# Optimization experiments

Hardware: AMD Instinct MI355X
Metric: run time of the kernel (lower is better)

The kernel has to match this reference:

```python
import math
import jax, jax.numpy as jnp
import numpy as np

B, T, D = 2, 1024, 512
H, DK = 8, 64


def setup_inputs() -> dict:
    key = jax.random.key(0)
    ks = jax.random.split(key, 7)
    s = 1.0 / math.sqrt(D)
    x = jax.random.normal(ks[0], (B, T, D), dtype=jnp.float32)
    Wq = jax.random.normal(ks[1], (D, H * DK), dtype=jnp.float32) * s
    Wk = jax.random.normal(ks[2], (D, H * DK), dtype=jnp.float32) * s
    Wv = jax.random.normal(ks[3], (D, H * DK), dtype=jnp.float32) * s
    Wo = jax.random.normal(ks[4], (H * DK, D), dtype=jnp.float32) * s
    Wg = jax.random.normal(ks[5], (D, H * DK), dtype=jnp.float32) * 0.02
    bg = jnp.ones((H * DK,), dtype=jnp.float32)  # gate_bias_init = 1.0
    return {"x": x, "Wq": Wq, "Wk": Wk, "Wv": Wv, "Wo": Wo, "Wg": Wg, "bg": bg}


def reference(x, Wq, Wk, Wv, Wo, Wg, bg):
    b, t, d = x.shape
    Q = jax.nn.relu(x @ Wq).reshape(b, t, H, DK)
    K = jax.nn.relu(x @ Wk).reshape(b, t, H, DK)
    V = (x @ Wv).reshape(b, t, H, DK)
    angle = jnp.arange(t, dtype=x.dtype) * (math.pi / (2 * t))  # (T,)
    cosw = jnp.cos(angle)[None, :, None, None]
    sinw = jnp.sin(angle)[None, :, None, None]
    Qc, Qs = Q * cosw, Q * sinw
    Kc, Ks = K * cosw, K * sinw
    # cumulative KV outer products: (B,T,H,DK,DK)
    Sc = jnp.cumsum(jnp.einsum('bthd,bthe->bthde', Kc, V), axis=1)
    Ss = jnp.cumsum(jnp.einsum('bthd,bthe->bthde', Ks, V), axis=1)
    o = jnp.einsum('bthd,bthde->bthe', Qc, Sc) + jnp.einsum('bthd,bthde->bthe', Qs, Ss)
    zc = jnp.cumsum(Kc, axis=1)
    zs = jnp.cumsum(Ks, axis=1)
    z = jnp.einsum('bthd,bthd->bth', Qc, zc) + jnp.einsum('bthd,bthd->bth', Qs, zs)
    z = jnp.maximum(z, 1e-6)[..., None]
    o = o / z
    gate = jax.nn.sigmoid((x @ Wg + bg).reshape(b, t, H, DK))
    o = o * gate
    return o.reshape(b, t, H * DK) @ Wo
```

## Files before the change

### kernel.cpp

```cpp
#include <hip/hip_runtime.h>
#include <math.h>

#define B_ 2
#define T_ 1024
#define D_ 512
#define H_ 8
#define DK_ 64
#define NBH_ 16
#define C_ 32
#define G_ 32

#define PI_OVER_2T 0.00153398078788564122971808758949f

typedef float f32x4 __attribute__((ext_vector_type(4)));
typedef short s16x8 __attribute__((ext_vector_type(8)));

__device__ __forceinline__ ushort f2bf(float x) {
    unsigned u = __float_as_uint(x);
    unsigned r = (u + 0x7fffu + ((u >> 16) & 1u)) >> 16;
    return (ushort)r;
}
__device__ __forceinline__ float bf2f(ushort u) {
    return __uint_as_float((unsigned)u << 16);
}
__device__ __forceinline__ s16x8 bscale(s16x8 v, float s) {
    s16x8 r;
#pragma unroll
    for (int u = 0; u < 8; u++)
        r[u] = (short)f2bf(bf2f((ushort)v[u]) * s);
    return r;
}

__device__ __forceinline__ void async16(void* lds, const void* g) {
    __builtin_amdgcn_global_load_lds(
        (const __attribute__((address_space(1))) void*)g,
        (__attribute__((address_space(3))) void*)lds, 16, 0, 0);
}

__global__ __launch_bounds__(256) void k_conv(
    const float* __restrict__ x,
    const float* __restrict__ Wq, const float* __restrict__ Wk,
    const float* __restrict__ Wv, const float* __restrict__ Wg,
    const float* __restrict__ Wo,
    ushort* __restrict__ xb, ushort* __restrict__ WtAll)
{
    __shared__ float Ts[64][65];
    const int bx = blockIdx.x;
    const int tid = threadIdx.x;
    if (bx < 1024) {
        int i = (bx * 256 + tid) * 4;
        float4 v = *(const float4*)&x[i];
        ushort4 o;
        o.x = f2bf(v.x); o.y = f2bf(v.y); o.z = f2bf(v.z); o.w = f2bf(v.w);
        *(ushort4*)&xb[i] = o;
        return;
    }
    const int bid = bx - 1024;
    const int mi = bid >> 6;
    const int t64 = bid & 63;
    const float* __restrict__ W = (mi == 0) ? Wq : (mi == 1) ? Wk
                                 : (mi == 2) ? Wv : (mi == 3) ? Wg : Wo;
    const int tr = t64 >> 3, tc = t64 & 7;
#pragma unroll
    for (int p = 0; p < 4; p++) {
        int row = p * 16 + (tid >> 4);
        int c4 = (tid & 15) * 4;
        float4 v = *(const float4*)&W[(size_t)(tr * 64 + row) * 512 + tc * 64 + c4];
        Ts[row][c4 + 0] = v.x; Ts[row][c4 + 1] = v.y;
        Ts[row][c4 + 2] = v.z; Ts[row][c4 + 3] = v.w;
    }
    __syncthreads();
    const int nl = tid >> 2, kc = (tid & 3) * 16;
    ushort buf[16];
#pragma unroll
    for (int u = 0; u < 16; u++) buf[u] = f2bf(Ts[kc + u][nl]);
    ushort* dst = WtAll + (size_t)mi * 262144 + (size_t)(tc * 64 + nl) * 512
                  + tr * 64 + kc;
    *(uint4*)dst = *(uint4*)&buf[0];
    *(uint4*)(dst + 8) = *(uint4*)&buf[8];
}

template<int MODE, int TM, int TN, int BK>
__global__ __launch_bounds__(256) void k_gemm(
    const ushort* __restrict__ A, const ushort* __restrict__ Bt,
    const float* __restrict__ bg,
    void* __restrict__ O0v, void* __restrict__ O1v,
    void* __restrict__ O2v, void* __restrict__ O3v)
{
    constexpr int WM = TM / 2, WN = TN / 2;
    constexpr int FM = WM / 16, FN = WN / 16;
    constexpr int CH = BK / 8;
    constexpr int SH = (BK == 32) ? 1 : 0;
    constexpr int KS = BK / 32;
    constexpr int NA = TM * BK / 2048;
    constexpr int NB = TN * BK / 2048;

    __shared__ ushort As[2][TM * BK];
    __shared__ ushort Bs[2][TN * BK];

    const int tid = threadIdx.x;
    const int ct = blockIdx.x;
    const int rowBase = blockIdx.y * TM;

    const ushort* __restrict__ Bmat;
    int which = 0, matCol;
    if (MODE == 0) {
        which = ct / (512 / TN);
        matCol = (ct % (512 / TN)) * TN;
        Bmat = Bt + (size_t)which * 262144;
    } else {
        matCol = ct * TN;
        Bmat = Bt;
    }

    const int wave = tid >> 6, lane = tid & 63;
    const int q = lane >> 4, ln = lane & 15;
    const int mB = (wave >> 1) * WM, nB = (wave & 1) * WN;

    int fuA[NA], fuB[NB];
    const ushort* gA[NA];
    const ushort* gB[NB];
#pragma unroll
    for (int u = 0; u < NA; u++) {
        int fu = tid * 8 + u * 2048;
        int r = fu / BK;
        int slot = (fu >> 3) & (CH - 1);
        int gc = slot ^ ((r >> SH) & (CH - 1));
        fuA[u] = fu;
        gA[u] = A + (size_t)(rowBase + r) * 512 + gc * 8;
    }
#pragma unroll
    for (int u = 0; u < NB; u++) {
        int fu = tid * 8 + u * 2048;
        int r = fu / BK;
        int slot = (fu >> 3) & (CH - 1);
        int gc = slot ^ ((r >> SH) & (CH - 1));
        fuB[u] = fu;
        gB[u] = Bmat + (size_t)(matCol + r) * 512 + gc * 8;
    }

    f32x4 acc[FM][FN];
#pragma unroll
    for (int i = 0; i < FM; i++)
#pragma unroll
        for (int j = 0; j < FN; j++) acc[i][j] = (f32x4){0.f, 0.f, 0.f, 0.f};

    int aoff[FM][KS], boff[FN][KS];
#pragma unroll
    for (int i = 0; i < FM; i++) {
        int ra = mB + i * 16 + ln;
#pragma unroll
        for (int ks = 0; ks < KS; ks++)
            aoff[i][ks] = ra * BK
                + (((ks * 4 + q) ^ ((ra >> SH) & (CH - 1))) * 8);
    }
#pragma unroll
    for (int j = 0; j < FN; j++) {
        int rb = nB + j * 16 + ln;
#pragma unroll
        for (int ks = 0; ks < KS; ks++)
            boff[j][ks] = rb * BK
                + (((ks * 4 + q) ^ ((rb >> SH) & (CH - 1))) * 8);
    }

#pragma unroll
    for (int u = 0; u < NA; u++) async16(&As[0][fuA[u]], gA[u]);
#pragma unroll
    for (int u = 0; u < NB; u++) async16(&Bs[0][fuB[u]], gB[u]);

    int cur = 0;
    for (int kb = 0; kb < 512; kb += BK) {
        __syncthreads();
        if (kb + BK < 512) {
#pragma unroll
            for (int u = 0; u < NA; u++)
                async16(&As[cur ^ 1][fuA[u]], gA[u] + kb + BK);
#pragma unroll
            for (int u = 0; u < NB; u++)
                async16(&Bs[cur ^ 1][fuB[u]], gB[u] + kb + BK);
        }
#pragma unroll
        for (int ks = 0; ks < KS; ks++) {
            s16x8 af[FM], bf[FN];
#pragma unroll
            for (int i = 0; i < FM; i++)
                af[i] = *(const s16x8*)&As[cur][aoff[i][ks]];
#pragma unroll
            for (int j = 0; j < FN; j++)
                bf[j] = *(const s16x8*)&Bs[cur][boff[j][ks]];
#pragma unroll
            for (int i = 0; i < FM; i++)
#pragma unroll
                for (int j = 0; j < FN; j++)
                    acc[i][j] = __builtin_amdgcn_mfma_f32_16x16x32_bf16(
                        af[i], bf[j], acc[i][j], 0, 0, 0);
        }
        cur ^= 1;
    }

    if (MODE == 0) {
        ushort* __restrict__ Out = (which == 0) ? (ushort*)O0v
                                  : (which == 1) ? (ushort*)O1v
                                  : (which == 2) ? (ushort*)O2v : (ushort*)O3v;
#pragma unroll
        for (int i = 0; i < FM; i++)
#pragma unroll
            for (int j = 0; j < FN; j++) {
                int col = matCol + nB + j * 16 + ln;
#pragma unroll
                for (int r = 0; r < 4; r++) {
                    int row = rowBase + mB + i * 16 + q * 4 + r;
                    float v = acc[i][j][r];
                    if (which <= 1) v = fmaxf(v, 0.f);
                    else if (which == 3) v = 1.f / (1.f + expf(-(v + bg[col])));
                    Out[(size_t)row * 512 + col] = f2bf(v);
                }
            }
    } else {
        float* __restrict__ Out = (float*)O0v;
#pragma unroll
        for (int i = 0; i < FM; i++)
#pragma unroll
            for (int j = 0; j < FN; j++) {
                int col = matCol + nB + j * 16 + ln;
#pragma unroll
                for (int r = 0; r < 4; r++) {
                    int row = rowBase + mB + i * 16 + q * 4 + r;
                    Out[(size_t)row * 512 + col] = acc[i][j][r];
                }
            }
    }
}

__global__ __launch_bounds__(256) void k_chunk_kv(
    const ushort* __restrict__ Kg, const ushort* __restrict__ Vg,
    ushort* __restrict__ Sst, float* __restrict__ Zst)
{
    __shared__ ushort KcT[64 * 40];
    __shared__ ushort KsT[64 * 40];
    __shared__ ushort VT [64 * 40];

    const int blk = blockIdx.x;
    const int bh = blk >> 5, g = blk & 31;
    const int b = bh >> 3, h = bh & 7;
    const int tid = threadIdx.x;
    const int rBase = b * T_ + g * C_;
    const int colB = h * DK_;

    {
        int row = tid >> 3, c8 = (tid & 7) * 8;
        float a = (float)(g * C_ + row) * PI_OVER_2T;
        float ca = cosf(a), sa = sinf(a);
        size_t ga = (size_t)(rBase + row) * D_ + colB + c8;
        uint4 kraw = *(const uint4*)&Kg[ga];
        uint4 vraw = *(const uint4*)&Vg[ga];
        const ushort* kp = (const ushort*)&kraw;
        const ushort* vp = (const ushort*)&vraw;
#pragma unroll
        for (int u = 0; u < 8; u++) {
            float kf = bf2f(kp[u]);
            KcT[(c8 + u) * 40 + row] = f2bf(kf * ca);
            KsT[(c8 + u) * 40 + row] = f2bf(kf * sa);
            VT [(c8 + u) * 40 + row] = vp[u];
        }
    }
    __syncthreads();

    if (tid < 128) {
        int d = tid & 63;
        const ushort* src = (tid < 64) ? KcT : KsT;
        float zsum = 0.f;
#pragma unroll
        for (int t = 0; t < C_; t++) zsum += bf2f(src[d * 40 + t]);
        Zst[(size_t)blk * 128 + tid] = zsum;
    }

    const int wave = tid >> 6, lane = tid & 63;
    const int q = lane >> 4, ln = lane & 15;
    s16x8 av = *(const s16x8*)&VT[(wave * 16 + ln) * 40 + q * 8];
    ushort* Sp = Sst + (size_t)blk * 8192;
#pragma unroll
    for (int nj = 0; nj < 4; nj++) {
        s16x8 bc = *(const s16x8*)&KcT[(nj * 16 + ln) * 40 + q * 8];
        s16x8 bs = *(const s16x8*)&KsT[(nj * 16 + ln) * 40 + q * 8];
        f32x4 ac = __builtin_amdgcn_mfma_f32_16x16x32_bf16(
            av, bc, (f32x4){0.f, 0.f, 0.f, 0.f}, 0, 0, 0);
        f32x4 as = __builtin_amdgcn_mfma_f32_16x16x32_bf16(
            av, bs, (f32x4){0.f, 0.f, 0.f, 0.f}, 0, 0, 0);
#pragma unroll
        for (int r = 0; r < 4; r++) {
            int e = wave * 16 + q * 4 + r;
            int d = nj * 16 + ln;
            Sp[e * 64 + d] = f2bf(ac[r]);
            Sp[4096 + e * 64 + d] = f2bf(as[r]);
        }
    }
}

__global__ __launch_bounds__(256) void k_scan(
    ushort* __restrict__ Sst, float* __restrict__ Zst)
{
    int id = blockIdx.x * 256 + threadIdx.x;
    if (id < 32768) {
        int bh = id >> 11, i4 = (id & 2047) * 4;
        size_t base = (size_t)bh * (G_ * 8192) + i4;
        ushort4 v[G_];
#pragma unroll
        for (int g = 0; g < G_; g++)
            v[g] = *(const ushort4*)&Sst[base + (size_t)g * 8192];
        float rx = 0.f, ry = 0.f, rz = 0.f, rw = 0.f;
#pragma unroll
        for (int g = 0; g < G_; g++) {
            ushort4 t = v[g];
            ushort4 o;
            o.x = f2bf(rx); o.y = f2bf(ry); o.z = f2bf(rz); o.w = f2bf(rw);
            *(ushort4*)&Sst[base + (size_t)g * 8192] = o;
            rx += bf2f(t.x); ry += bf2f(t.y);
            rz += bf2f(t.z); rw += bf2f(t.w);
        }
    } else {
        int id2 = id - 32768;
        if (id2 >= 512) return;
        int bh = id2 >> 5, i4 = (id2 & 31) * 4;
        size_t base = (size_t)bh * (G_ * 128) + i4;
        float4 v[G_];
#pragma unroll
        for (int g = 0; g < G_; g++)
            v[g] = *(const float4*)&Zst[base + (size_t)g * 128];
        float4 run = make_float4(0.f, 0.f, 0.f, 0.f);
#pragma unroll
        for (int g = 0; g < G_; g++) {
            float4 t = v[g];
            *(float4*)&Zst[base + (size_t)g * 128] = run;
            run.x += t.x; run.y += t.y; run.z += t.z; run.w += t.w;
        }
    }
}

__global__ __launch_bounds__(256) void k_out_chunk(
    const ushort* __restrict__ Qg, const ushort* __restrict__ Kg,
    const ushort* __restrict__ Vg, const ushort* __restrict__ Gg,
    const ushort* __restrict__ Sst, const float* __restrict__ Zst,
    ushort* __restrict__ Op)
{
    __shared__ ushort VT[64 * 40];
    __shared__ ushort Pb[32 * 40];
    __shared__ float zinv[32];

    const int blk = blockIdx.x;
    const int bh = blk >> 5, g = blk & 31;
    const int b = bh >> 3, h = bh & 7;
    const int tid = threadIdx.x;
    const int rBase = b * T_ + g * C_;
    const int colB = h * DK_;
    const int wave = tid >> 6, lane = tid & 63;
    const int q = lane >> 4, ln = lane & 15;

    {
        int row = tid >> 3, c8 = (tid & 7) * 8;
        uint4 vraw = *(const uint4*)&Vg[(size_t)(rBase + row) * D_ + colB + c8];
        const ushort* vp = (const ushort*)&vraw;
#pragma unroll
        for (int u = 0; u < 8; u++) VT[(c8 + u) * 40 + row] = vp[u];
    }

    const int mi = wave >> 1, njp = wave & 1;
    const ushort* qrow = Qg + (size_t)(rBase + mi * 16 + ln) * D_ + colB;
    s16x8 aq0 = *(const s16x8*)&qrow[q * 8];
    s16x8 aq1 = *(const s16x8*)&qrow[32 + q * 8];
    {
        const ushort* krow = Kg + (size_t)(rBase + njp * 16 + ln) * D_ + colB;
        s16x8 bk0 = *(const s16x8*)&krow[q * 8];
        s16x8 bk1 = *(const s16x8*)&krow[32 + q * 8];
        f32x4 pacc = __builtin_amdgcn_mfma_f32_16x16x32_bf16(
            aq0, bk0, (f32x4){0.f, 0.f, 0.f, 0.f}, 0, 0, 0);
        pacc = __builtin_amdgcn_mfma_f32_16x16x32_bf16(aq1, bk1, pacc, 0, 0, 0);
        int sl = njp * 16 + ln;
        float as_ = (float)(g * C_ + sl) * PI_OVER_2T;
        float cs_ = cosf(as_), ss_ = sinf(as_);
#pragma unroll
        for (int r = 0; r < 4; r++) {
            int tl = mi * 16 + q * 4 + r;
            float at = (float)(g * C_ + tl) * PI_OVER_2T;
            float w = (sl <= tl) ? (cosf(at) * cs_ + sinf(at) * ss_) : 0.f;
            Pb[tl * 40 + sl] = f2bf(pacc[r] * w);
        }
    }
    __syncthreads();

    {
        int t = tid >> 3, sub = tid & 7;
        uint4 qraw = *(const uint4*)&Qg[(size_t)(rBase + t) * D_ + colB + sub * 8];
        const ushort* qp = (const ushort*)&qraw;
        const float* zcp = Zst + (size_t)blk * 128 + sub * 8;
        float4 zc0 = *(const float4*)&zcp[0];
        float4 zc1 = *(const float4*)&zcp[4];
        float4 zs0 = *(const float4*)&zcp[64];
        float4 zs1 = *(const float4*)&zcp[68];
        float pc = 0.f, ps = 0.f;
        float zcv[8] = {zc0.x, zc0.y, zc0.z, zc0.w, zc1.x, zc1.y, zc1.z, zc1.w};
        float zsv[8] = {zs0.x, zs0.y, zs0.z, zs0.w, zs1.x, zs1.y, zs1.z, zs1.w};
#pragma unroll
        for (int u = 0; u < 8; u++) {
            float qf = bf2f(qp[u]);
            pc += qf * zcv[u]; ps += qf * zsv[u];
        }
        float pr = 0.f;
#pragma unroll
        for (int u = 0; u < 4; u++) pr += bf2f(Pb[t * 40 + sub * 4 + u]);
#pragma unroll
        for (int m = 1; m < 8; m <<= 1) {
            pc += __shfl_xor(pc, m);
            ps += __shfl_xor(ps, m);
            pr += __shfl_xor(pr, m);
        }
        if (sub == 0) {
            float at = (float)(g * C_ + t) * PI_OVER_2T;
            float z = cosf(at) * pc + sinf(at) * ps + pr;
            zinv[t] = 1.f / fmaxf(z, 1e-6f);
        }
    }
    __syncthreads();

    {
        float am = (float)(g * C_ + mi * 16 + ln) * PI_OVER_2T;
        float cm = cosf(am), sm = sinf(am);
        s16x8 aqc0 = bscale(aq0, cm), aqc1 = bscale(aq1, cm);
        s16x8 aqs0 = bscale(aq0, sm), aqs1 = bscale(aq1, sm);
        s16x8 pf = *(const s16x8*)&Pb[(mi * 16 + ln) * 40 + q * 8];
        const ushort* Sp = Sst + (size_t)blk * 8192;
#pragma unroll
        for (int jj = 0; jj < 2; jj++) {
            int nj = 2 * (wave & 1) + jj;
            const ushort* scp = Sp + (nj * 16 + ln) * 64;
            s16x8 bc0 = *(const s16x8*)&scp[q * 8];
            s16x8 bc1 = *(const s16x8*)&scp[32 + q * 8];
            s16x8 bs0 = *(const s16x8*)&scp[4096 + q * 8];
            s16x8 bs1 = *(const s16x8*)&scp[4096 + 32 + q * 8];
            s16x8 bv  = *(const s16x8*)&VT[(nj * 16 + ln) * 40 + q * 8];
            f32x4 acc = __builtin_amdgcn_mfma_f32_16x16x32_bf16(
                pf, bv, (f32x4){0.f, 0.f, 0.f, 0.f}, 0, 0, 0);
            acc = __builtin_amdgcn_mfma_f32_16x16x32_bf16(aqc0, bc0, acc, 0, 0, 0);
            acc = __builtin_amdgcn_mfma_f32_16x16x32_bf16(aqc1, bc1, acc, 0, 0, 0);
            acc = __builtin_amdgcn_mfma_f32_16x16x32_bf16(aqs0, bs0, acc, 0, 0, 0);
            acc = __builtin_amdgcn_mfma_f32_16x16x32_bf16(aqs1, bs1, acc, 0, 0, 0);
#pragma unroll
            for (int r = 0; r < 4; r++) {
                int tl = mi * 16 + q * 4 + r;
                int e = nj * 16 + ln;
                size_t go = (size_t)(rBase + tl) * D_ + colB + e;
                float o = acc[r] * zinv[tl] * bf2f(Gg[go]);
                Op[go] = f2bf(o);
            }
        }
    }
}

extern "C" void kernel_launch(void* const* d_in, const int* in_sizes, int n_in,
                              void* d_out, int out_size, void* d_ws, size_t ws_size,
                              hipStream_t stream)
{
    const float* x  = (const float*)d_in[0];
    const float* Wq = (const float*)d_in[1];
    const float* Wk = (const float*)d_in[2];
    const float* Wv = (const float*)d_in[3];
    const float* Wo = (const float*)d_in[4];
    const float* Wg = (const float*)d_in[5];
    const float* bg = (const float*)d_in[6];
    float* out = (float*)d_out;

    ushort* wsu = (ushort*)d_ws;
    ushort* xb    = wsu;
    ushort* WtAll = xb + 1048576;
    ushort* Qg    = WtAll + 1310720;
    ushort* Kg    = Qg + 1048576;
    ushort* Vg    = Kg + 1048576;
    ushort* Gg    = Vg + 1048576;
    ushort* Sst   = Gg + 1048576;
    ushort* Opb   = Sst + 4194304;
    float*  Zst   = (float*)(Opb + 1048576);

    dim3 blk(256);
    k_conv<<<dim3(1344), blk, 0, stream>>>(x, Wq, Wk, Wv, Wg, Wo, xb, WtAll);
    k_gemm<0, 128, 64, 64><<<dim3(32, 16), blk, 0, stream>>>(
        xb, WtAll, bg, Qg, Kg, Vg, Gg);
    k_chunk_kv<<<dim3(NBH_ * G_), blk, 0, stream>>>(Kg, Vg, Sst, Zst);
    k_scan<<<dim3(130), blk, 0, stream>>>(Sst, Zst);
    k_out_chunk<<<dim3(NBH_ * G_), blk, 0, stream>>>(
        Qg, Kg, Vg, Gg, Sst, Zst, Opb);
    k_gemm<1, 64, 64, 64><<<dim3(8, 32), blk, 0, stream>>>(
        Opb, WtAll + (size_t)4 * 262144, nullptr, out, nullptr, nullptr, nullptr);
}
```

Baseline: 113.7 us.

## Fuse K/V projection GEMM with per-chunk KV state computation

Replaces the QKVG projection GEMM and the separate chunk-KV kernel with one kernel. Each block computes two matching column tiles, either Q and gate or K and V for one head. K/V blocks then build the cos/sin-weighted chunk states and Z sums directly from their accumulators in shared memory. This removes a kernel launch and the re-read of K and V from global memory. In exchange the tiles are smaller (64 rows), the kernel uses more shared memory through a union, and K/V blocks carry an extra epilogue, which may unbalance the grid.

Result: faster. 104.9 us (-7.8%).

```diff
diff --git a/kernel.cpp b/kernel.cpp
--- a/kernel.cpp
+++ b/kernel.cpp
@@ -80,6 +80,209 @@
     *(uint4*)(dst + 8) = *(uint4*)&buf[8];
 }
 
+__global__ __launch_bounds__(256) void k_g0(
+    const ushort* __restrict__ A, const ushort* __restrict__ WtAll,
+    const float* __restrict__ bg,
+    ushort* __restrict__ Qg, ushort* __restrict__ Kg,
+    ushort* __restrict__ Vg, ushort* __restrict__ Gg,
+    ushort* __restrict__ Sst, float* __restrict__ Zst)
+{
+    __shared__ union {
+        struct { ushort As[2][64 * 64]; ushort Bs[2][2 * 64 * 64]; } s;
+        struct { ushort KcT[64 * 72]; ushort KsT[64 * 72];
+                 ushort VT[64 * 72]; } e;
+    } sm;
+
+    const int tid = threadIdx.x;
+    const int ct = blockIdx.x;
+    const int rowBase = blockIdx.y * 64;
+    const bool isKV = (ct >= 8);
+    const int matCol = (ct & 7) * 64;
+    const ushort* __restrict__ B0 = WtAll + (size_t)(isKV ? 1 : 0) * 262144;
+    const ushort* __restrict__ B1 = WtAll + (size_t)(isKV ? 2 : 3) * 262144;
+
+    const int wave = tid >> 6, lane = tid & 63;
+    const int q = lane >> 4, ln = lane & 15;
+    const int mB = (wave >> 1) * 32, nB = (wave & 1) * 32;
+
+    int fu[2];
+    const ushort* gA[2];
+    const ushort* gB0[2];
+    const ushort* gB1[2];
+#pragma unroll
+    for (int u = 0; u < 2; u++) {
+        int f = tid * 8 + u * 2048;
+        int r = f >> 6;
+        int gc = ((f >> 3) & 7) ^ (r & 7);
+        fu[u] = f;
+        gA[u]  = A  + (size_t)(rowBase + r) * 512 + gc * 8;
+        gB0[u] = B0 + (size_t)(matCol + r) * 512 + gc * 8;
+        gB1[u] = B1 + (size_t)(matCol + r) * 512 + gc * 8;
+    }
+
+    f32x4 accA[2][2], accB[2][2];
+#pragma unroll
+    for (int i = 0; i < 2; i++)
+#pragma unroll
+        for (int j = 0; j < 2; j++) {
+            accA[i][j] = (f32x4){0.f, 0.f, 0.f, 0.f};
+            accB[i][j] = (f32x4){0.f, 0.f, 0.f, 0.f};
+        }
+
+    int aoff[2][2], boff[2][2];
+#pragma unroll
+    for (int i = 0; i < 2; i++) {
+        int ra = mB + i * 16 + ln;
+#pragma unroll
+        for (int ks = 0; ks < 2; ks++)
+            aoff[i][ks] = ra * 64 + (((ks * 4 + q) ^ (ra & 7)) * 8);
+    }
+#pragma unroll
+    for (int j = 0; j < 2; j++) {
+        int rb = nB + j * 16 + ln;
+#pragma unroll
+        for (int ks = 0; ks < 2; ks++)
+            boff[j][ks] = rb * 64 + (((ks * 4 + q) ^ (rb & 7)) * 8);
+    }
+
+#pragma unroll
+    for (int u = 0; u < 2; u++) {
+        async16(&sm.s.As[0][fu[u]], gA[u]);
+        async16(&sm.s.Bs[0][fu[u]], gB0[u]);
+        async16(&sm.s.Bs[0][4096 + fu[u]], gB1[u]);
+    }
+
+    int cur = 0;
+    for (int kb = 0; kb < 512; kb += 64) {
+        __syncthreads();
+        if (kb + 64 < 512) {
+            int nxt = cur ^ 1;
+#pragma unroll
+            for (int u = 0; u < 2; u++) {
+                async16(&sm.s.As[nxt][fu[u]], gA[u] + kb + 64);
+                async16(&sm.s.Bs[nxt][fu[u]], gB0[u] + kb + 64);
+                async16(&sm.s.Bs[nxt][4096 + fu[u]], gB1[u] + kb + 64);
+            }
+        }
+#pragma unroll
+        for (int ks = 0; ks < 2; ks++) {
+            s16x8 af[2], b0f[2], b1f[2];
+#pragma unroll
+            for (int i = 0; i < 2; i++)
+                af[i] = *(const s16x8*)&sm.s.As[cur][aoff[i][ks]];
+#pragma unroll
+            for (int j = 0; j < 2; j++) {
+                b0f[j] = *(const s16x8*)&sm.s.Bs[cur][boff[j][ks]];
+                b1f[j] = *(const s16x8*)&sm.s.Bs[cur][4096 + boff[j][ks]];
+            }
+#pragma unroll
+            for (int i = 0; i < 2; i++)
+#pragma unroll
+                for (int j = 0; j < 2; j++) {
+                    accA[i][j] = __builtin_amdgcn_mfma_f32_16x16x32_bf16(
+                        af[i], b0f[j], accA[i][j], 0, 0, 0);
+                    accB[i][j] = __builtin_amdgcn_mfma_f32_16x16x32_bf16(
+                        af[i], b1f[j], accB[i][j], 0, 0, 0);
+                }
+        }
+        cur ^= 1;
+    }
+    __syncthreads();
+
+    if (!isKV) {
+#pragma unroll
+        for (int i = 0; i < 2; i++)
+#pragma unroll
+            for (int j = 0; j < 2; j++) {
+                int col = matCol + nB + j * 16 + ln;
+#pragma unroll
+                for (int r = 0; r < 4; r++) {
+                    int row = rowBase + mB + i * 16 + q * 4 + r;
+                    Qg[(size_t)row * 512 + col] = f2bf(fmaxf(accA[i][j][r], 0.f));
+                    Gg[(size_t)row * 512 + col] =
+                        f2bf(1.f / (1.f + expf(-(accB[i][j][r] + bg[col]))));
+                }
+            }
+        return;
+    }
+
+    const int h = ct - 8;
+    const int b = rowBase >> 10;
+    const int c = wave >> 1;
+    const int gG = ((rowBase & 1023) >> 5) + c;
+    const int blk = (b * 8 + h) * 32 + gG;
+
+    float zc[2] = {0.f, 0.f}, zs[2] = {0.f, 0.f};
+#pragma unroll
+    for (int i = 0; i < 2; i++)
+#pragma unroll
+        for (int r = 0; r < 4; r++) {
+            int tLoc = mB + i * 16 + q * 4 + r;
+            int rowG = rowBase + tLoc;
+            float a = (float)(rowG & 1023) * PI_OVER_2T;
+            float ca = cosf(a), sa = sinf(a);
+#pragma unroll
+            for (int j = 0; j < 2; j++) {
+                int col = nB + j * 16 + ln;
+                float kv = fmaxf(accA[i][j][r], 0.f);
+                float vv = accB[i][j][r];
+                size_t go = (size_t)rowG * 512 + h * 64 + col;
+                Kg[go] = f2bf(kv);
+                Vg[go] = f2bf(vv);
+                float kc = kv * ca, ks = kv * sa;
+                sm.e.KcT[col * 72 + tLoc] = f2bf(kc);
+                sm.e.KsT[col * 72 + tLoc] = f2bf(ks);
+                sm.e.VT [col * 72 + tLoc] = f2bf(vv);
+                zc[j] += kc; zs[j] += ks;
+            }
+        }
+#pragma unroll
+    for (int j = 0; j < 2; j++) {
+        zc[j] += __shfl_xor(zc[j], 16); zc[j] += __shfl_xor(zc[j], 32);
+        zs[j] += __shfl_xor(zs[j], 16); zs[j] += __shfl_xor(zs[j], 32);
+    }
+    if (q == 0) {
+#pragma unroll
+        for (int j = 0; j < 2; j++) {
+            int d = nB + j * 16 + ln;
+            Zst[(size_t)blk * 128 + d] = zc[j];
+            Zst[(size_t)blk * 128 + 64 + d] = zs[j];
+        }
+    }
+    __syncthreads();
+
+    {
+        const int eh = (wave & 1) * 32;
+        ushort* Sp = Sst + (size_t)blk * 8192;
+        s16x8 av[2];
+#pragma unroll
+        for (int fi = 0; fi < 2; fi++)
+            av[fi] = *(const s16x8*)&sm.e.VT[(eh + fi * 16 + ln) * 72
+                                            + c * 32 + q * 8];
+#pragma unroll
+        for (int fj = 0; fj < 4; fj++) {
+            s16x8 bc = *(const s16x8*)&sm.e.KcT[(fj * 16 + ln) * 72
+                                                + c * 32 + q * 8];
+            s16x8 bs = *(const s16x8*)&sm.e.KsT[(fj * 16 + ln) * 72
+                                                + c * 32 + q * 8];
+#pragma unroll
+            for (int fi = 0; fi < 2; fi++) {
+                f32x4 sc = __builtin_amdgcn_mfma_f32_16x16x32_bf16(
+                    av[fi], bc, (f32x4){0.f, 0.f, 0.f, 0.f}, 0, 0, 0);
+                f32x4 ss = __builtin_amdgcn_mfma_f32_16x16x32_bf16(
+                    av[fi], bs, (f32x4){0.f, 0.f, 0.f, 0.f}, 0, 0, 0);
+#pragma unroll
+                for (int rr = 0; rr < 4; rr++) {
+                    int e = eh + fi * 16 + q * 4 + rr;
+                    int d = fj * 16 + ln;
+                    Sp[e * 64 + d] = f2bf(sc[rr]);
+                    Sp[4096 + e * 64 + d] = f2bf(ss[rr]);
+                }
+            }
+        }
+    }
+}
+
 template<int MODE, int TM, int TN, int BK>
 __global__ __launch_bounds__(256) void k_gemm(
     const ushort* __restrict__ A, const ushort* __restrict__ Bt,
@@ -102,16 +305,8 @@
     const int ct = blockIdx.x;
     const int rowBase = blockIdx.y * TM;
 
-    const ushort* __restrict__ Bmat;
-    int which = 0, matCol;
-    if (MODE == 0) {
-        which = ct / (512 / TN);
-        matCol = (ct % (512 / TN)) * TN;
-        Bmat = Bt + (size_t)which * 262144;
-    } else {
-        matCol = ct * TN;
-        Bmat = Bt;
-    }
+    const int matCol = ct * TN;
+    const ushort* __restrict__ Bmat = Bt;
 
     const int wave = tid >> 6, lane = tid & 63;
     const int q = lane >> 4, ln = lane & 15;
@@ -151,16 +346,14 @@
         int ra = mB + i * 16 + ln;
 #pragma unroll
         for (int ks = 0; ks < KS; ks++)
-            aoff[i][ks] = ra * BK
-                + (((ks * 4 + q) ^ ((ra >> SH) & (CH - 1))) * 8);
+            aoff[i][ks] = ra * BK + (((ks * 4 + q) ^ ((ra >> SH) & (CH - 1))) * 8);
     }
 #pragma unroll
     for (int j = 0; j < FN; j++) {
         int rb = nB + j * 16 + ln;
 #pragma unroll
         for (int ks = 0; ks < KS; ks++)
-            boff[j][ks] = rb * BK
-                + (((ks * 4 + q) ^ ((rb >> SH) & (CH - 1))) * 8);
+            boff[j][ks] = rb * BK + (((ks * 4 + q) ^ ((rb >> SH) & (CH - 1))) * 8);
     }
 
 #pragma unroll
@@ -198,103 +391,18 @@
         cur ^= 1;
     }
 
-    if (MODE == 0) {
-        ushort* __restrict__ Out = (which == 0) ? (ushort*)O0v
-                                  : (which == 1) ? (ushort*)O1v
-                                  : (which == 2) ? (ushort*)O2v : (ushort*)O3v;
-#pragma unroll
-        for (int i = 0; i < FM; i++)
-#pragma unroll
-            for (int j = 0; j < FN; j++) {
-                int col = matCol + nB + j * 16 + ln;
-#pragma unroll
-                for (int r = 0; r < 4; r++) {
-                    int row = rowBase + mB + i * 16 + q * 4 + r;
-                    float v = acc[i][j][r];
-                    if (which <= 1) v = fmaxf(v, 0.f);
-                    else if (which == 3) v = 1.f / (1.f + expf(-(v + bg[col])));
-                    Out[(size_t)row * 512 + col] = f2bf(v);
-                }
+    float* __restrict__ Out = (float*)O0v;
+#pragma unroll
+    for (int i = 0; i < FM; i++)
+#pragma unroll
+        for (int j = 0; j < FN; j++) {
+            int col = matCol + nB + j * 16 + ln;
+#pragma unroll
+            for (int r = 0; r < 4; r++) {
+                int row = rowBase + mB + i * 16 + q * 4 + r;
+                Out[(size_t)row * 512 + col] = acc[i][j][r];
             }
-    } else {
-        float* __restrict__ Out = (float*)O0v;
-#pragma unroll
-        for (int i = 0; i < FM; i++)
-#pragma unroll
-            for (int j = 0; j < FN; j++) {
-                int col = matCol + nB + j * 16 + ln;
-#pragma unroll
-                for (int r = 0; r < 4; r++) {
-                    int row = rowBase + mB + i * 16 + q * 4 + r;
-                    Out[(size_t)row * 512 + col] = acc[i][j][r];
-                }
-            }
-    }
-}
-
-__global__ __launch_bounds__(256) void k_chunk_kv(
-    const ushort* __restrict__ Kg, const ushort* __restrict__ Vg,
-    ushort* __restrict__ Sst, float* __restrict__ Zst)
-{
-    __shared__ ushort KcT[64 * 40];
-    __shared__ ushort KsT[64 * 40];
-    __shared__ ushort VT [64 * 40];
-
-    const int blk = blockIdx.x;
-    const int bh = blk >> 5, g = blk & 31;
-    const int b = bh >> 3, h = bh & 7;
-    const int tid = threadIdx.x;
-    const int rBase = b * T_ + g * C_;
-    const int colB = h * DK_;
-
-    {
-        int row = tid >> 3, c8 = (tid & 7) * 8;
-        float a = (float)(g * C_ + row) * PI_OVER_2T;
-        float ca = cosf(a), sa = sinf(a);
-        size_t ga = (size_t)(rBase + row) * D_ + colB + c8;
-        uint4 kraw = *(const uint4*)&Kg[ga];
-        uint4 vraw = *(const uint4*)&Vg[ga];
-        const ushort* kp = (const ushort*)&kraw;
-        const ushort* vp = (const ushort*)&vraw;
-#pragma unroll
-        for (int u = 0; u < 8; u++) {
-            float kf = bf2f(kp[u]);
-            KcT[(c8 + u) * 40 + row] = f2bf(kf * ca);
-            KsT[(c8 + u) * 40 + row] = f2bf(kf * sa);
-            VT [(c8 + u) * 40 + row] = vp[u];
-        }
-    }
-    __syncthreads();
-
-    if (tid < 128) {
-        int d = tid & 63;
-        const ushort* src = (tid < 64) ? KcT : KsT;
-        float zsum = 0.f;
-#pragma unroll
-        for (int t = 0; t < C_; t++) zsum += bf2f(src[d * 40 + t]);
-        Zst[(size_t)blk * 128 + tid] = zsum;
-    }
-
-    const int wave = tid >> 6, lane = tid & 63;
-    const int q = lane >> 4, ln = lane & 15;
-    s16x8 av = *(const s16x8*)&VT[(wave * 16 + ln) * 40 + q * 8];
-    ushort* Sp = Sst + (size_t)blk * 8192;
-#pragma unroll
-    for (int nj = 0; nj < 4; nj++) {
-        s16x8 bc = *(const s16x8*)&KcT[(nj * 16 + ln) * 40 + q * 8];
-        s16x8 bs = *(const s16x8*)&KsT[(nj * 16 + ln) * 40 + q * 8];
-        f32x4 ac = __builtin_amdgcn_mfma_f32_16x16x32_bf16(
-            av, bc, (f32x4){0.f, 0.f, 0.f, 0.f}, 0, 0, 0);
-        f32x4 as = __builtin_amdgcn_mfma_f32_16x16x32_bf16(
-            av, bs, (f32x4){0.f, 0.f, 0.f, 0.f}, 0, 0, 0);
-#pragma unroll
-        for (int r = 0; r < 4; r++) {
-            int e = wave * 16 + q * 4 + r;
-            int d = nj * 16 + ln;
-            Sp[e * 64 + d] = f2bf(ac[r]);
-            Sp[4096 + e * 64 + d] = f2bf(as[r]);
-        }
-    }
+        }
 }
 
 __global__ __launch_bounds__(256) void k_scan(
@@ -424,9 +532,9 @@
 
     {
         float am = (float)(g * C_ + mi * 16 + ln) * PI_OVER_2T;
-        float cm = cosf(am), sm = sinf(am);
+        float cm = cosf(am), sm_ = sinf(am);
         s16x8 aqc0 = bscale(aq0, cm), aqc1 = bscale(aq1, cm);
-        s16x8 aqs0 = bscale(aq0, sm), aqs1 = bscale(aq1, sm);
+        s16x8 aqs0 = bscale(aq0, sm_), aqs1 = bscale(aq1, sm_);
         s16x8 pf = *(const s16x8*)&Pb[(mi * 16 + ln) * 40 + q * 8];
         const ushort* Sp = Sst + (size_t)blk * 8192;
 #pragma unroll
@@ -482,12 +590,12 @@
 
     dim3 blk(256);
     k_conv<<<dim3(1344), blk, 0, stream>>>(x, Wq, Wk, Wv, Wg, Wo, xb, WtAll);
-    k_gemm<0, 128, 64, 64><<<dim3(32, 16), blk, 0, stream>>>(
-        xb, WtAll, bg, Qg, Kg, Vg, Gg);
-    k_chunk_kv<<<dim3(NBH_ * G_), blk, 0, stream>>>(Kg, Vg, Sst, Zst);
+    k_g0<<<dim3(16, 32), blk, 0, stream>>>(
+        xb, WtAll, bg, Qg, Kg, Vg, Gg, Sst, Zst);
     k_scan<<<dim3(130), blk, 0, stream>>>(Sst, Zst);
     k_out_chunk<<<dim3(NBH_ * G_), blk, 0, stream>>>(
         Qg, Kg, Vg, Gg, Sst, Zst, Opb);
     k_gemm<1, 64, 64, 64><<<dim3(8, 32), blk, 0, stream>>>(
-        Opb, WtAll + (size_t)4 * 262144, nullptr, out, nullptr, nullptr, nullptr);
-}
+        Opb, WtAll + (size_t)4 * 262144, nullptr,
+        out, nullptr, nullptr, nullptr);
+}
```
